# Kernel optimization log

Measured on AMD Instinct MI355X. Metric: run time of the kernel, lower is better.

Reference implementation:

```python
import jax, jax.numpy as jnp
import numpy as np

K = 5            # srn kernel size (kernels[0])
EPSILON = 1e-3   # epsilons -> SRN additive noise scale
BN_EPS = 1e-5
NUM_SLICES = 3
OUT_CH = 64
CLASSES = 5


def _unfold(x, k):
    # torch.nn.Unfold, padding=0: (B, C*k*k, L), channel-major then (kh, kw) row-major
    B, C, H, W = x.shape
    Ho, Wo = H - k + 1, W - k + 1
    cols = jnp.stack([x[:, :, i:i + Ho, j:j + Wo]
                      for i in range(k) for j in range(k)], axis=2)  # (B,C,k*k,Ho,Wo)
    return cols.reshape(B, C * k * k, Ho * Wo), Ho, Wo


def _bn(x, g, b):
    # BatchNorm2d in training mode: batch statistics, biased variance
    m = x.mean((0, 2, 3), keepdims=True)
    v = x.var((0, 2, 3), keepdims=True)
    return (x - m) * jax.lax.rsqrt(v + BN_EPS) * g[None, :, None, None] + b[None, :, None, None]


def _conv(x, w, b):
    y = jax.lax.conv_general_dilated(x, w, (1, 1), 'VALID',
                                     dimension_numbers=('NCHW', 'OIHW', 'NCHW'))
    return y + b[None, :, None, None]


def _avgpool(x, s):
    B, C, H, W = x.shape
    return x.reshape(B, C, H // s, s, W // s, s).mean((3, 5))


def _maxpool(x, s):
    B, C, H, W = x.shape
    return x.reshape(B, C, H // s, s, W // s, s).max((3, 5))


def _srn(x, srn_w):
    B = x.shape[0]
    y, Ho, Wo = _unfold(x, K)                               # (B, n, L)
    y = y + EPSILON * jax.random.normal(jax.random.key(42), y.shape, y.dtype)
    gg = jnp.std(y, axis=1, ddof=1, keepdims=True)          # torch.std is unbiased
    y = y / gg
    O, C, _, _, S = srn_w.shape
    n = C * K * K
    X = srn_w.reshape(O, n, S)
    X = jnp.concatenate([jnp.ones((O, n, 1), X.dtype), X], axis=2)   # (O, n, S+1)
    Xcov = jnp.einsum('onf,ong->ofg', X, X)                 # X^T X, (O, 4, 4)
    Xinv = jnp.linalg.inv(Xcov)
    M = jnp.einsum('ofg,ong->ofn', Xinv, X)
    Wc = jnp.einsum('ofn,bnl->bofl', M, y)
    pred = jnp.einsum('onf,bofl->bonl', X, Wc)              # fitted values (B,O,n,L)
    err = jnp.mean((y[:, None] - pred) ** 2, axis=2)        # (B,O,L)
    err = err.reshape(B, O, Ho, Wo)
    A = (jnp.exp(-err) - np.exp(-1.0)) / (1.0 - np.exp(-1.0))
    return A - 0.5


def setup_inputs() -> dict:
    key = jax.random.key(0)
    ks = jax.random.split(key, 12)
    x = jax.random.normal(ks[0], (4, 3, 64, 64), jnp.float32)
    # xavier-style init scaled up for numerical stability of the small-matrix inverse
    srn_w = 0.05 * jax.random.normal(ks[1], (OUT_CH, 3, K, K, NUM_SLICES), jnp.float32)
    conv2_w = 0.05 * jax.random.normal(ks[2], (128, 64, 3, 3), jnp.float32)
    conv2_b = 0.01 * jax.random.normal(ks[3], (128,), jnp.float32)
    conv3_w = 0.05 * jax.random.normal(ks[4], (128, 128, 3, 3), jnp.float32)
    conv3_b = 0.01 * jax.random.normal(ks[5], (128,), jnp.float32)
    conv4_w = 0.05 * jax.random.normal(ks[6], (128, 128, 3, 3), jnp.float32)
    conv4_b = 0.01 * jax.random.normal(ks[7], (128,), jnp.float32)
    bn1_g = jnp.ones((64,), jnp.float32); bn1_b = jnp.zeros((64,), jnp.float32)
    bn2_g = jnp.ones((128,), jnp.float32); bn2_b = jnp.zeros((128,), jnp.float32)
    bn3_g = jnp.ones((128,), jnp.float32); bn3_b = jnp.zeros((128,), jnp.float32)
    bn4_g = jnp.ones((128,), jnp.float32); bn4_b = jnp.zeros((128,), jnp.float32)
    fc2_w = 0.05 * jax.random.normal(ks[8], (CLASSES, 128, 1, 1), jnp.float32)
    fc2_b = 0.01 * jax.random.normal(ks[9], (CLASSES,), jnp.float32)
    return dict(x=x, srn_w=srn_w, conv2_w=conv2_w, conv2_b=conv2_b,
                conv3_w=conv3_w, conv3_b=conv3_b, conv4_w=conv4_w, conv4_b=conv4_b,
                bn1_g=bn1_g, bn1_b=bn1_b, bn2_g=bn2_g, bn2_b=bn2_b,
                bn3_g=bn3_g, bn3_b=bn3_b, bn4_g=bn4_g, bn4_b=bn4_b,
                fc2_w=fc2_w, fc2_b=fc2_b)


def reference(x, srn_w, conv2_w, conv2_b, conv3_w, conv3_b, conv4_w, conv4_b,
              bn1_g, bn1_b, bn2_g, bn2_b, bn3_g, bn3_b, bn4_g, bn4_b,
              fc2_w, fc2_b):
    h = _srn(x, srn_w)                                      # (B,64,60,60)
    h = _avgpool(h, 2)
    h = _bn(h, bn1_g, bn1_b)
    h = jax.nn.relu(_bn(_conv(h, conv2_w, conv2_b), bn2_g, bn2_b))
    h = _avgpool(h, 2)
    h = jax.nn.relu(_bn(_conv(h, conv3_w, conv3_b), bn3_g, bn3_b))
    h = _maxpool(h, 2)
    h = jax.nn.relu(_bn(_conv(h, conv4_w, conv4_b), bn4_g, bn4_b))
    h = _maxpool(h, 4)                                      # (B,128,1,1)
    flat = h.reshape(h.shape[0], -1)                        # (B,128)
    return flat @ fc2_w.reshape(CLASSES, -1).T + fc2_b      # 1x1 conv == matmul
```

## Files before the change

### kernel.cpp

```cpp
#include <hip/hip_runtime.h>
#include <math.h>

__device__ __align__(16) float g_G[64 * 16];
__device__ __align__(16) float g_Wp[64 * 240];
__device__ __align__(16) float g_w2p[9 * 2304 * 4];
__device__ __align__(16) float g_w3p[17 * 2304 * 4];
__device__ __align__(16) float g_w4p[8 * 4608 * 4];
__device__ float g_s1[64],  g_q1[64];
__device__ float g_s2[128], g_q2[128];
__device__ float g_s3[128], g_q3[128];
__device__ float g_s4[128], g_q4[128];
__device__ __align__(16) float g_h1[4 * 30 * 30 * 64];
__device__ __align__(16) float g_h2[4 * 14 * 14 * 4 * 128];
__device__ __align__(16) float g_h3[4 * 6 * 6 * 4 * 128];
__device__ __align__(16) float g_h4[4 * 16 * 128];

__global__ void k_prep(const float* __restrict__ srn_w, const float* __restrict__ w2,
                       const float* __restrict__ w3, const float* __restrict__ w4) {
    int t = threadIdx.x, bid = blockIdx.x;
    int gid = bid * 256 + t, gstride = 128 * 256;
    for (int i = gid; i < 14400; i += gstride) {
        int o = i / 225, j = i % 225, row = j / 15, col = j % 15;
        g_Wp[o * 240 + row * 16 + col] = srn_w[i];
    }
    for (int j = gid; j < 73728; j += gstride) {
        int c = j & 3, s4 = j >> 2;
        int sl = s4 % 36, tmp = s4 / 36, oc_l = tmp & 63, blk = tmp >> 6;
        int it = blk & 3, ocg = blk >> 2;
        int kw = sl % 3, icq = (sl / 3) & 3, kh = sl / 12;
        int ic = it * 16 + icq * 4 + c;
        g_w2p[j] = w2[((ocg * 64 + oc_l) * 64 + ic) * 9 + kh * 3 + kw];
    }
    for (int j = gid; j < 147456; j += gstride) {
        int c = j & 3, s4 = j >> 2;
        int sl = s4 % 36, tmp = s4 / 36, oc_l = tmp & 63, blk = tmp >> 6;
        int it = blk & 7, ocg = blk >> 3;
        int kw = sl % 3, icq = (sl / 3) & 3, kh = sl / 12;
        int ic = it * 16 + icq * 4 + c;
        g_w3p[j] = w3[((ocg * 64 + oc_l) * 128 + ic) * 9 + kh * 3 + kw];
    }
    for (int j = gid; j < 147456; j += gstride) {
        int c = j & 3, s4 = j >> 2;
        int sl = s4 % 72, tmp = s4 / 72, oc_l = tmp & 15, blkq = tmp >> 4;
        int icq = blkq & 3, ocg = blkq >> 2;
        int kw = sl % 3, icb = (sl / 3) & 7, kh = sl / 24;
        int ic = icq * 32 + icb * 4 + c;
        g_w4p[j] = w4[((ocg * 16 + oc_l) * 128 + ic) * 9 + kh * 3 + kw];
    }
    if (bid == 0) {
        if (t < 64) { g_s1[t] = 0.f; g_q1[t] = 0.f; }
        if (t < 128) {
            g_s2[t] = 0.f; g_q2[t] = 0.f;
            g_s3[t] = 0.f; g_q3[t] = 0.f;
            g_s4[t] = 0.f; g_q4[t] = 0.f;
        }
        if (t < 64) {
            int o = t;
            const float* w = srn_w + o * 225;
            float c01 = 0, c02 = 0, c03 = 0, c11 = 0, c12 = 0, c13 = 0,
                  c22 = 0, c23 = 0, c33 = 0;
            for (int n = 0; n < 75; n++) {
                float w1 = w[n * 3 + 0], w2v = w[n * 3 + 1], w3v = w[n * 3 + 2];
                c01 += w1; c02 += w2v; c03 += w3v;
                c11 += w1 * w1; c12 += w1 * w2v; c13 += w1 * w3v;
                c22 += w2v * w2v; c23 += w2v * w3v; c33 += w3v * w3v;
            }
            float A[4][8];
            A[0][0] = 75.f; A[0][1] = c01; A[0][2] = c02; A[0][3] = c03;
            A[1][0] = c01;  A[1][1] = c11; A[1][2] = c12; A[1][3] = c13;
            A[2][0] = c02;  A[2][1] = c12; A[2][2] = c22; A[2][3] = c23;
            A[3][0] = c03;  A[3][1] = c13; A[3][2] = c23; A[3][3] = c33;
            for (int i = 0; i < 4; i++)
                for (int j = 0; j < 4; j++) A[i][4 + j] = (i == j) ? 1.f : 0.f;
            for (int p = 0; p < 4; p++) {
                float ip = 1.f / A[p][p];
                for (int j = 0; j < 8; j++) A[p][j] *= ip;
                for (int i = 0; i < 4; i++) if (i != p) {
                    float f = A[i][p];
                    for (int j = 0; j < 8; j++) A[i][j] -= f * A[p][j];
                }
            }
            for (int i = 0; i < 4; i++)
                for (int j = 0; j < 4; j++) g_G[o * 16 + i * 4 + j] = A[i][4 + j];
        }
    }
}

__global__ __launch_bounds__(256) void k_srn(const float* __restrict__ x) {
    __shared__ __align__(16) float wlds[64 * 244];
    __shared__ __align__(16) float glds[64 * 20];
    __shared__ float xsm[648];
    __shared__ float part[2 * 15 * 66];
    __shared__ float redS[256], redQ[256];
    int blk = blockIdx.x;
    int b = blk / 60, rem = blk % 60, r = rem >> 1, ch = rem & 1;
    int t = threadIdx.x;

    float4 wreg[15];
#pragma unroll
    for (int k = 0; k < 15; k++) wreg[k] = ((const float4*)g_Wp)[k * 256 + t];
    float4 greg = ((const float4*)g_G)[t];
    float xr[3];
#pragma unroll
    for (int k = 0; k < 3; k++) {
        int i = t + k * 256;
        if (i < 648) {
            int c = i / 216, rm = i % 216, rr = rm / 36, col = rm % 36;
            int gc = ch * 30 + col; if (gc > 63) gc = 63;
            xr[k] = x[((b * 3 + c) * 64 + (2 * r + rr)) * 64 + gc];
        }
    }
#pragma unroll
    for (int k = 0; k < 15; k++) {
        int idx = k * 256 + t;
        *(float4*)&wlds[(idx / 60) * 244 + (idx % 60) * 4] = wreg[k];
    }
    *(float4*)&glds[(t >> 2) * 20 + (t & 3) * 4] = greg;
#pragma unroll
    for (int k = 0; k < 3; k++) { int i = t + k * 256; if (i < 648) xsm[i] = xr[k]; }
    __syncthreads();

    int w = t >> 6, o = t & 63;
    int rw = w & 1, cq = w >> 1, base = cq * 16;

    float z1[16], z2[16], z3[16], s[16], q[16];
#pragma unroll
    for (int i = 0; i < 16; i++) { z1[i] = 0; z2[i] = 0; z3[i] = 0; s[i] = 0; q[i] = 0; }

    for (int c = 0; c < 3; c++) {
#pragma unroll
        for (int kh = 0; kh < 5; kh++) {
            float xv[20];
#pragma unroll
            for (int k = 0; k < 20; k++) xv[k] = xsm[(c * 6 + rw + kh) * 36 + base + k];
            float wf[16];
            const float* wp = &wlds[o * 244 + (c * 5 + kh) * 16];
            *(float4*)&wf[0]  = *(const float4*)&wp[0];
            *(float4*)&wf[4]  = *(const float4*)&wp[4];
            *(float4*)&wf[8]  = *(const float4*)&wp[8];
            *(float4*)&wf[12] = *(const float4*)&wp[12];
#pragma unroll
            for (int kw = 0; kw < 5; kw++) {
                float w1 = wf[kw * 3], w2 = wf[kw * 3 + 1], w3 = wf[kw * 3 + 2];
#pragma unroll
                for (int i = 0; i < 16; i++) {
                    float v = xv[kw + i];
                    s[i] += v; q[i] += v * v;
                    z1[i] += w1 * v; z2[i] += w2 * v; z3[i] += w3 * v;
                }
            }
        }
    }

    float gm[16];
    {
        const float* gp = &glds[o * 20];
        *(float4*)&gm[0]  = *(const float4*)&gp[0];
        *(float4*)&gm[4]  = *(const float4*)&gp[4];
        *(float4*)&gm[8]  = *(const float4*)&gp[8];
        *(float4*)&gm[12] = *(const float4*)&gp[12];
    }
    const float C1 = 0.36787944117144233f;
    const float INV = 1.5819767068693265f;
#pragma unroll
    for (int pp = 0; pp < 8; pp++) {
        int pl = cq * 8 + pp;
        if (pl < 15) {
            float aa = 0.f;
#pragma unroll
            for (int e = 0; e < 2; e++) {
                int i = 2 * pp + e;
                float sum = s[i], sq = q[i];
                float gg2 = (sq - sum * sum * (1.f / 75.f)) * (1.f / 74.f);
                float zf[4] = { sum, z1[i], z2[i], z3[i] };
                float qf = 0.f;
#pragma unroll
                for (int f = 0; f < 4; f++) {
                    float acc = 0.f;
#pragma unroll
                    for (int h = 0; h < 4; h++) acc += gm[f * 4 + h] * zf[h];
                    qf += acc * zf[f];
                }
                float err = (sq - qf) / (75.f * gg2);
                aa += (expf(-err) - C1) * INV - 0.5f;
            }
            part[(rw * 15 + pl) * 66 + o] = 0.25f * aa;
        }
    }
    __syncthreads();

    int j = t >> 6;
    float ps = 0.f, pq = 0.f;
    for (int pl = j; pl < 15; pl += 4) {
        float v = part[pl * 66 + o] + part[(15 + pl) * 66 + o];
        g_h1[((b * 30 + r) * 30 + ch * 15 + pl) * 64 + o] = v;
        ps += v; pq += v * v;
    }
    redS[t] = ps; redQ[t] = pq;
    __syncthreads();
    if (t < 64) {
        atomicAdd(&g_s1[t], redS[t] + redS[64 + t] + redS[128 + t] + redS[192 + t]);
        atomicAdd(&g_q1[t], redQ[t] + redQ[64 + t] + redQ[128 + t] + redQ[192 + t]);
    }
}

__global__ __launch_bounds__(256) void k_conv2(const float* __restrict__ g1,
                                               const float* __restrict__ b1) {
    __shared__ __align__(16) float ws[64 * 148];
    __shared__ __align__(16) float xs[3 * 30 * 64];
    __shared__ float redS[256], redQ[256];
    int blk = blockIdx.x;
    int b = blk / 56, rem = blk % 56, oh = rem >> 1, ocg = rem & 1;
    int t = threadIdx.x;
    int oc_l = t & 63, qtr = t >> 6, owb = qtr * 7;

    {
        int icb = (t & 15) * 4;
        float4 S = *(const float4*)&g_s1[icb], Q = *(const float4*)&g_q1[icb];
        float4 G4 = *(const float4*)&g1[icb], B4 = *(const float4*)&b1[icb];
        float scv[4], shv[4];
        float mm[4] = { S.x, S.y, S.z, S.w }, qq[4] = { Q.x, Q.y, Q.z, Q.w };
        float gg[4] = { G4.x, G4.y, G4.z, G4.w }, bb[4] = { B4.x, B4.y, B4.z, B4.w };
#pragma unroll
        for (int c = 0; c < 4; c++) {
            float m = mm[c] * (1.f / 3600.f);
            float v = qq[c] * (1.f / 3600.f) - m * m;
            scv[c] = gg[c] * rsqrtf(v + 1e-5f);
            shv[c] = bb[c] - m * scv[c];
        }
        const float4* src4 = (const float4*)(g_h1 + (b * 900 + oh * 30) * 64);
        float4 xr[6];
#pragma unroll
        for (int k = 0; k < 6; k++) { int i4 = t + k * 256; if (i4 < 1440) xr[k] = src4[i4]; }
        const float4* wsrc0 = (const float4*)g_w2p;
        float4 wreg[9];
#pragma unroll
        for (int k = 0; k < 9; k++) wreg[k] = wsrc0[(ocg * 4) * 2304 + k * 256 + t];
#pragma unroll
        for (int k = 0; k < 6; k++) {
            int i4 = t + k * 256;
            if (i4 < 1440) {
                float4 v;
                v.x = xr[k].x * scv[0] + shv[0]; v.y = xr[k].y * scv[1] + shv[1];
                v.z = xr[k].z * scv[2] + shv[2]; v.w = xr[k].w * scv[3] + shv[3];
                *(float4*)&xs[i4 * 4] = v;
            }
        }
#pragma unroll
        for (int k = 0; k < 9; k++) {
            int idx = k * 256 + t;
            *(float4*)&ws[(idx / 36) * 148 + (idx % 36) * 4] = wreg[k];
        }
    }
    __syncthreads();

    float acc[7] = {0, 0, 0, 0, 0, 0, 0};
    const float4* wsrc = (const float4*)g_w2p + (ocg * 4) * 2304;
    for (int it = 0; it < 4; ++it) {
        float4 wreg[9];
        if (it < 3) {
#pragma unroll
            for (int k = 0; k < 9; k++) wreg[k] = wsrc[(it + 1) * 2304 + k * 256 + t];
        }
#pragma unroll 1
        for (int icq = 0; icq < 4; icq++) {
            int xoff = it * 16 + icq * 4;
#pragma unroll
            for (int kh = 0; kh < 3; kh++) {
                const float* wb = &ws[oc_l * 148 + (kh * 4 + icq) * 12];
                float4 w0 = *(const float4*)&wb[0];
                float4 w1 = *(const float4*)&wb[4];
                float4 w2v = *(const float4*)&wb[8];
                const float* xrow = &xs[(kh * 30 + owb) * 64 + xoff];
                float4 x0 = *(const float4*)&xrow[0];
                float4 x1 = *(const float4*)&xrow[64];
#pragma unroll
                for (int i = 0; i < 7; i++) {
                    float4 x2 = *(const float4*)&xrow[(i + 2) * 64];
                    acc[i] += w0.x * x0.x + w0.y * x0.y + w0.z * x0.z + w0.w * x0.w
                            + w1.x * x1.x + w1.y * x1.y + w1.z * x1.z + w1.w * x1.w
                            + w2v.x * x2.x + w2v.y * x2.y + w2v.z * x2.z + w2v.w * x2.w;
                    x0 = x1; x1 = x2;
                }
            }
        }
        if (it < 3) {
            __syncthreads();
#pragma unroll
            for (int k = 0; k < 9; k++) {
                int idx = k * 256 + t;
                *(float4*)&ws[(idx / 36) * 148 + (idx % 36) * 4] = wreg[k];
            }
            __syncthreads();
        }
    }
    int oc = ocg * 64 + oc_l;
    float ps = 0.f, pq = 0.f;
#pragma unroll
    for (int i = 0; i < 7; i++) {
        int ow = owb + i;
        g_h2[(((b * 14 + (oh >> 1)) * 14 + (ow >> 1)) * 4 + (oh & 1) * 2 + (ow & 1)) * 128 + oc] = acc[i];
        ps += acc[i]; pq += acc[i] * acc[i];
    }
    redS[t] = ps; redQ[t] = pq;
    __syncthreads();
    if (t < 64) {
        atomicAdd(&g_s2[ocg * 64 + t], redS[t] + redS[64 + t] + redS[128 + t] + redS[192 + t]);
        atomicAdd(&g_q2[ocg * 64 + t], redQ[t] + redQ[64 + t] + redQ[128 + t] + redQ[192 + t]);
    }
}

__global__ __launch_bounds__(256) void k_conv3(const float* __restrict__ g2,
                                               const float* __restrict__ b2) {
    __shared__ __align__(16) float ws[64 * 148];
    __shared__ __align__(16) float xs[3 * 14 * 128];
    __shared__ float redS[256], redQ[256];
    int blk = blockIdx.x;
    int b = blk / 24, rem = blk % 24, oh = rem >> 1, ocg = rem & 1;
    int t = threadIdx.x;
    int oc_l = t & 63, qtr = t >> 6, owb = qtr * 3;

    {
        int icb = (t & 31) * 4;
        float4 S = *(const float4*)&g_s2[icb], Q = *(const float4*)&g_q2[icb];
        float4 G4 = *(const float4*)&g2[icb], B4 = *(const float4*)&b2[icb];
        float scv[4], shv[4];
        float mm[4] = { S.x, S.y, S.z, S.w }, qq[4] = { Q.x, Q.y, Q.z, Q.w };
        float gg[4] = { G4.x, G4.y, G4.z, G4.w }, bb[4] = { B4.x, B4.y, B4.z, B4.w };
#pragma unroll
        for (int c = 0; c < 4; c++) {
            float m = mm[c] * (1.f / 3136.f);
            float v = qq[c] * (1.f / 3136.f) - m * m;
            scv[c] = gg[c] * rsqrtf(v + 1e-5f);
            shv[c] = bb[c] - m * scv[c];
        }
        const float4* wsrc0 = (const float4*)g_w3p;
        float4 wreg[9];
#pragma unroll
        for (int k = 0; k < 9; k++) wreg[k] = wsrc0[(ocg * 8) * 2304 + k * 256 + t];
        float4 va[6], vb[6], vc[6], vd[6];
#pragma unroll
        for (int k = 0; k < 6; k++) {
            int i4 = t + k * 256;
            if (i4 < 1344) {
                int px = (i4 >> 5) % 14, rr = i4 / 448;
                const float4* p0 = (const float4*)&g_h2[(((b * 14 + oh + rr) * 14 + px) * 4) * 128 + (i4 & 31) * 4];
                va[k] = p0[0]; vb[k] = p0[32]; vc[k] = p0[64]; vd[k] = p0[96];
            }
        }
#pragma unroll
        for (int k = 0; k < 9; k++) {
            int idx = k * 256 + t;
            *(float4*)&ws[(idx / 36) * 148 + (idx % 36) * 4] = wreg[k];
        }
#pragma unroll
        for (int k = 0; k < 6; k++) {
            int i4 = t + k * 256;
            if (i4 < 1344) {
                float4 o4;
                o4.x = 0.25f * (fmaxf(va[k].x * scv[0] + shv[0], 0.f) + fmaxf(vb[k].x * scv[0] + shv[0], 0.f)
                              + fmaxf(vc[k].x * scv[0] + shv[0], 0.f) + fmaxf(vd[k].x * scv[0] + shv[0], 0.f));
                o4.y = 0.25f * (fmaxf(va[k].y * scv[1] + shv[1], 0.f) + fmaxf(vb[k].y * scv[1] + shv[1], 0.f)
                              + fmaxf(vc[k].y * scv[1] + shv[1], 0.f) + fmaxf(vd[k].y * scv[1] + shv[1], 0.f));
                o4.z = 0.25f * (fmaxf(va[k].z * scv[2] + shv[2], 0.f) + fmaxf(vb[k].z * scv[2] + shv[2], 0.f)
                              + fmaxf(vc[k].z * scv[2] + shv[2], 0.f) + fmaxf(vd[k].z * scv[2] + shv[2], 0.f));
                o4.w = 0.25f * (fmaxf(va[k].w * scv[3] + shv[3], 0.f) + fmaxf(vb[k].w * scv[3] + shv[3], 0.f)
                              + fmaxf(vc[k].w * scv[3] + shv[3], 0.f) + fmaxf(vd[k].w * scv[3] + shv[3], 0.f));
                *(float4*)&xs[i4 * 4] = o4;
            }
        }
    }
    __syncthreads();

    float acc[3] = {0, 0, 0};
    const float4* wsrc = (const float4*)g_w3p + (ocg * 8) * 2304;
    for (int it = 0; it < 8; ++it) {
        float4 wreg[9];
        if (it < 7) {
#pragma unroll
            for (int k = 0; k < 9; k++) wreg[k] = wsrc[(it + 1) * 2304 + k * 256 + t];
        }
#pragma unroll 1
        for (int icq = 0; icq < 4; icq++) {
            int xoff = it * 16 + icq * 4;
#pragma unroll
            for (int kh = 0; kh < 3; kh++) {
                const float* wb = &ws[oc_l * 148 + (kh * 4 + icq) * 12];
                float4 w0 = *(const float4*)&wb[0];
                float4 w1 = *(const float4*)&wb[4];
                float4 w2v = *(const float4*)&wb[8];
                const float* xrow = &xs[(kh * 14 + owb) * 128 + xoff];
                float4 x0 = *(const float4*)&xrow[0];
                float4 x1 = *(const float4*)&xrow[128];
#pragma unroll
                for (int i = 0; i < 3; i++) {
                    float4 x2 = *(const float4*)&xrow[(i + 2) * 128];
                    acc[i] += w0.x * x0.x + w0.y * x0.y + w0.z * x0.z + w0.w * x0.w
                            + w1.x * x1.x + w1.y * x1.y + w1.z * x1.z + w1.w * x1.w
                            + w2v.x * x2.x + w2v.y * x2.y + w2v.z * x2.z + w2v.w * x2.w;
                    x0 = x1; x1 = x2;
                }
            }
        }
        if (it < 7) {
            __syncthreads();
#pragma unroll
            for (int k = 0; k < 9; k++) {
                int idx = k * 256 + t;
                *(float4*)&ws[(idx / 36) * 148 + (idx % 36) * 4] = wreg[k];
            }
            __syncthreads();
        }
    }
    int oc = ocg * 64 + oc_l;
    float ps = 0.f, pq = 0.f;
#pragma unroll
    for (int i = 0; i < 3; i++) {
        int ow = owb + i;
        g_h3[(((b * 6 + (oh >> 1)) * 6 + (ow >> 1)) * 4 + (oh & 1) * 2 + (ow & 1)) * 128 + oc] = acc[i];
        ps += acc[i]; pq += acc[i] * acc[i];
    }
    redS[t] = ps; redQ[t] = pq;
    __syncthreads();
    if (t < 64) {
        atomicAdd(&g_s3[ocg * 64 + t], redS[t] + redS[64 + t] + redS[128 + t] + redS[192 + t]);
        atomicAdd(&g_q3[ocg * 64 + t], redQ[t] + redQ[64 + t] + redQ[128 + t] + redQ[192 + t]);
    }
}

__global__ __launch_bounds__(256) void k_conv4(const float* __restrict__ g3,
                                               const float* __restrict__ b3) {
    __shared__ __align__(16) float ws[64 * 292];
    __shared__ __align__(16) float xs[3 * 6 * 128];
    __shared__ float red[256];
    int blk = blockIdx.x;
    int b = blk / 32, rem = blk % 32, oh = rem / 8, ocg = rem % 8;
    int t = threadIdx.x;
    int oc_l = t & 15, ow = (t >> 4) & 3, icq = t >> 6;

    {
        int icb = (t & 31) * 4;
        float4 S = *(const float4*)&g_s3[icb], Q = *(const float4*)&g_q3[icb];
        float4 G4 = *(const float4*)&g3[icb], B4 = *(const float4*)&b3[icb];
        float scv[4], shv[4];
        float mm[4] = { S.x, S.y, S.z, S.w }, qq[4] = { Q.x, Q.y, Q.z, Q.w };
        float gg[4] = { G4.x, G4.y, G4.z, G4.w }, bb[4] = { B4.x, B4.y, B4.z, B4.w };
#pragma unroll
        for (int c = 0; c < 4; c++) {
            float m = mm[c] * (1.f / 576.f);
            float v = qq[c] * (1.f / 576.f) - m * m;
            scv[c] = gg[c] * rsqrtf(v + 1e-5f);
            shv[c] = bb[c] - m * scv[c];
        }
        const float4* wsrc = (const float4*)g_w4p + ocg * 4608;
        float4 wreg[18];
#pragma unroll
        for (int k = 0; k < 18; k++) wreg[k] = wsrc[k * 256 + t];
        float4 va[3], vb[3], vc[3], vd[3];
#pragma unroll
        for (int k = 0; k < 3; k++) {
            int i4 = t + k * 256;
            if (i4 < 576) {
                int px = (i4 >> 5) % 6, rr = i4 / 192;
                const float4* p0 = (const float4*)&g_h3[(((b * 6 + oh + rr) * 6 + px) * 4) * 128 + (i4 & 31) * 4];
                va[k] = p0[0]; vb[k] = p0[32]; vc[k] = p0[64]; vd[k] = p0[96];
            }
        }
#pragma unroll
        for (int k = 0; k < 18; k++) {
            int idx = k * 256 + t;
            *(float4*)&ws[(idx / 72) * 292 + (idx % 72) * 4] = wreg[k];
        }
#pragma unroll
        for (int k = 0; k < 3; k++) {
            int i4 = t + k * 256;
            if (i4 < 576) {
                float4 o4;
                o4.x = fmaxf(fmaxf(fmaxf(va[k].x * scv[0] + shv[0], vb[k].x * scv[0] + shv[0]),
                                   fmaxf(vc[k].x * scv[0] + shv[0], vd[k].x * scv[0] + shv[0])), 0.f);
                o4.y = fmaxf(fmaxf(fmaxf(va[k].y * scv[1] + shv[1], vb[k].y * scv[1] + shv[1]),
                                   fmaxf(vc[k].y * scv[1] + shv[1], vd[k].y * scv[1] + shv[1])), 0.f);
                o4.z = fmaxf(fmaxf(fmaxf(va[k].z * scv[2] + shv[2], vb[k].z * scv[2] + shv[2]),
                                   fmaxf(vc[k].z * scv[2] + shv[2], vd[k].z * scv[2] + shv[2])), 0.f);
                o4.w = fmaxf(fmaxf(fmaxf(va[k].w * scv[3] + shv[3], vb[k].w * scv[3] + shv[3]),
                                   fmaxf(vc[k].w * scv[3] + shv[3], vd[k].w * scv[3] + shv[3])), 0.f);
                *(float4*)&xs[i4 * 4] = o4;
            }
        }
    }
    __syncthreads();

    float acc = 0.f;
    const float* wbase = &ws[(icq * 16 + oc_l) * 292];
#pragma unroll 1
    for (int icbq = 0; icbq < 8; icbq++) {
#pragma unroll
        for (int kh = 0; kh < 3; kh++) {
            const float* wb = &wbase[(kh * 8 + icbq) * 12];
            float4 w0 = *(const float4*)&wb[0];
            float4 w1 = *(const float4*)&wb[4];
            float4 w2v = *(const float4*)&wb[8];
            float4 x0 = *(const float4*)&xs[(kh * 6 + ow) * 128 + icq * 32 + icbq * 4];
            float4 x1 = *(const float4*)&xs[(kh * 6 + ow + 1) * 128 + icq * 32 + icbq * 4];
            float4 x2 = *(const float4*)&xs[(kh * 6 + ow + 2) * 128 + icq * 32 + icbq * 4];
            acc += w0.x * x0.x + w0.y * x0.y + w0.z * x0.z + w0.w * x0.w
                 + w1.x * x1.x + w1.y * x1.y + w1.z * x1.z + w1.w * x1.w
                 + w2v.x * x2.x + w2v.y * x2.y + w2v.z * x2.z + w2v.w * x2.w;
        }
    }
    red[t] = acc;
    __syncthreads();
    if (t < 64) {
        float v = red[t] + red[t + 64] + red[t + 128] + red[t + 192];
        int oc = ocg * 16 + (t & 15);
        g_h4[((b * 4 + oh) * 4 + (t >> 4)) * 128 + oc] = v;
        float ps = v + __shfl_xor(v, 16);  ps += __shfl_xor(ps, 32);
        float pv = v * v;
        float pq = pv + __shfl_xor(pv, 16); pq += __shfl_xor(pq, 32);
        if (t < 16) { atomicAdd(&g_s4[ocg * 16 + t], ps); atomicAdd(&g_q4[ocg * 16 + t], pq); }
    }
}

__global__ __launch_bounds__(256) void k_final(const float* __restrict__ g4,
                                               const float* __restrict__ b4,
                                               const float* __restrict__ fcw,
                                               const float* __restrict__ fcb,
                                               float* __restrict__ out) {
    __shared__ float sc[128], sh[128];
    __shared__ float pooled[4][128];
    int t = threadIdx.x;
    if (t < 128) {
        float m = g_s4[t] * (1.f / 64.f);
        float v = g_q4[t] * (1.f / 64.f) - m * m;
        float rs = rsqrtf(v + 1e-5f);
        sc[t] = g4[t] * rs; sh[t] = b4[t] - m * sc[t];
    }
    __syncthreads();
    for (int item = t; item < 512; item += 256) {
        int b = item >> 7, oc = item & 127;
        float s = sc[oc], h = sh[oc];
        float mx = 0.f;
#pragma unroll
        for (int k = 0; k < 16; k++) mx = fmaxf(mx, g_h4[(b * 16 + k) * 128 + oc] * s + h);
        pooled[b][oc] = mx;
    }
    __syncthreads();
    if (t < 20) {
        int b = t / 5, cls = t % 5;
        float acc = fcb[cls];
        const float* w = &fcw[cls * 128];
        for (int oc = 0; oc < 128; oc++) acc += pooled[b][oc] * w[oc];
        out[b * 5 + cls] = acc;
    }
}

extern "C" void kernel_launch(void* const* d_in, const int* in_sizes, int n_in,
                              void* d_out, int out_size, void* d_ws, size_t ws_size,
                              hipStream_t stream) {
    (void)in_sizes; (void)n_in; (void)out_size; (void)d_ws; (void)ws_size;
    const float* x     = (const float*)d_in[0];
    const float* srn_w = (const float*)d_in[1];
    const float* w2    = (const float*)d_in[2];
    const float* w3    = (const float*)d_in[4];
    const float* w4    = (const float*)d_in[6];
    const float* g1 = (const float*)d_in[8];  const float* b1 = (const float*)d_in[9];
    const float* g2 = (const float*)d_in[10]; const float* b2 = (const float*)d_in[11];
    const float* g3 = (const float*)d_in[12]; const float* b3 = (const float*)d_in[13];
    const float* g4 = (const float*)d_in[14]; const float* b4 = (const float*)d_in[15];
    const float* fcw = (const float*)d_in[16]; const float* fcb = (const float*)d_in[17];
    float* out = (float*)d_out;

    k_prep <<<dim3(128), dim3(256), 0, stream>>>(srn_w, w2, w3, w4);
    k_srn  <<<dim3(240), dim3(256), 0, stream>>>(x);
    k_conv2<<<dim3(224), dim3(256), 0, stream>>>(g1, b1);
    k_conv3<<<dim3(96),  dim3(256), 0, stream>>>(g2, b2);
    k_conv4<<<dim3(128), dim3(256), 0, stream>>>(g3, b3);
    k_final<<<dim3(1),   dim3(256), 0, stream>>>(g4, b4, fcw, fcb, out);
}
```

Measured before the change: 115.4 us.

## Fold weight-prep kernel into downstream stages and zero BN stats via memset

Removes the separate k_prep launch. Each weight repack now runs inside the kernel one stage earlier: w2 in k_srn, w3 in k_conv2, w4 in k_conv3. Every SRN block computes its own 4x4 Gram inverse from the weights it holds in LDS. The BN statistic accumulators move to the workspace and are cleared with hipMemsetAsync. This saves a launch and its serialization, but adds redundant per-block Gram work and extra global writes in kernels that were already busy. The memset is still a separate stream operation.

Result: faster. 111.2 us (-3.7%).

```diff
diff --git a/kernel.cpp b/kernel.cpp
--- a/kernel.cpp
+++ b/kernel.cpp
@@ -1,29 +1,26 @@
 #include <hip/hip_runtime.h>
 #include <math.h>
 
-__device__ __align__(16) float g_G[64 * 16];
-__device__ __align__(16) float g_Wp[64 * 240];
 __device__ __align__(16) float g_w2p[9 * 2304 * 4];
 __device__ __align__(16) float g_w3p[17 * 2304 * 4];
 __device__ __align__(16) float g_w4p[8 * 4608 * 4];
-__device__ float g_s1[64],  g_q1[64];
-__device__ float g_s2[128], g_q2[128];
-__device__ float g_s3[128], g_q3[128];
-__device__ float g_s4[128], g_q4[128];
 __device__ __align__(16) float g_h1[4 * 30 * 30 * 64];
 __device__ __align__(16) float g_h2[4 * 14 * 14 * 4 * 128];
 __device__ __align__(16) float g_h3[4 * 6 * 6 * 4 * 128];
 __device__ __align__(16) float g_h4[4 * 16 * 128];
 
-__global__ void k_prep(const float* __restrict__ srn_w, const float* __restrict__ w2,
-                       const float* __restrict__ w3, const float* __restrict__ w4) {
-    int t = threadIdx.x, bid = blockIdx.x;
-    int gid = bid * 256 + t, gstride = 128 * 256;
-    for (int i = gid; i < 14400; i += gstride) {
-        int o = i / 225, j = i % 225, row = j / 15, col = j % 15;
-        g_Wp[o * 240 + row * 16 + col] = srn_w[i];
-    }
-    for (int j = gid; j < 73728; j += gstride) {
+__global__ __launch_bounds__(256) void k_srn(const float* __restrict__ x,
+                                             const float* __restrict__ srn_w,
+                                             const float* __restrict__ w2,
+                                             float* __restrict__ stats) {
+    __shared__ __align__(16) float wlds[64 * 244];
+    __shared__ float xsm[648];
+    __shared__ float part[2 * 15 * 66];
+    __shared__ float redS[256], redQ[256];
+    int bid = blockIdx.x, t = threadIdx.x;
+    int b = bid / 60, rem = bid % 60, r = rem >> 1, ch = rem & 1;
+
+    for (int j = bid * 256 + t; j < 73728; j += 240 * 256) {
         int c = j & 3, s4 = j >> 2;
         int sl = s4 % 36, tmp = s4 / 36, oc_l = tmp & 63, blk = tmp >> 6;
         int it = blk & 3, ocg = blk >> 2;
@@ -31,75 +28,13 @@
         int ic = it * 16 + icq * 4 + c;
         g_w2p[j] = w2[((ocg * 64 + oc_l) * 64 + ic) * 9 + kh * 3 + kw];
     }
-    for (int j = gid; j < 147456; j += gstride) {
-        int c = j & 3, s4 = j >> 2;
-        int sl = s4 % 36, tmp = s4 / 36, oc_l = tmp & 63, blk = tmp >> 6;
-        int it = blk & 7, ocg = blk >> 3;
-        int kw = sl % 3, icq = (sl / 3) & 3, kh = sl / 12;
-        int ic = it * 16 + icq * 4 + c;
-        g_w3p[j] = w3[((ocg * 64 + oc_l) * 128 + ic) * 9 + kh * 3 + kw];
-    }
-    for (int j = gid; j < 147456; j += gstride) {
-        int c = j & 3, s4 = j >> 2;
-        int sl = s4 % 72, tmp = s4 / 72, oc_l = tmp & 15, blkq = tmp >> 4;
-        int icq = blkq & 3, ocg = blkq >> 2;
-        int kw = sl % 3, icb = (sl / 3) & 7, kh = sl / 24;
-        int ic = icq * 32 + icb * 4 + c;
-        g_w4p[j] = w4[((ocg * 16 + oc_l) * 128 + ic) * 9 + kh * 3 + kw];
-    }
-    if (bid == 0) {
-        if (t < 64) { g_s1[t] = 0.f; g_q1[t] = 0.f; }
-        if (t < 128) {
-            g_s2[t] = 0.f; g_q2[t] = 0.f;
-            g_s3[t] = 0.f; g_q3[t] = 0.f;
-            g_s4[t] = 0.f; g_q4[t] = 0.f;
-        }
-        if (t < 64) {
-            int o = t;
-            const float* w = srn_w + o * 225;
-            float c01 = 0, c02 = 0, c03 = 0, c11 = 0, c12 = 0, c13 = 0,
-                  c22 = 0, c23 = 0, c33 = 0;
-            for (int n = 0; n < 75; n++) {
-                float w1 = w[n * 3 + 0], w2v = w[n * 3 + 1], w3v = w[n * 3 + 2];
-                c01 += w1; c02 += w2v; c03 += w3v;
-                c11 += w1 * w1; c12 += w1 * w2v; c13 += w1 * w3v;
-                c22 += w2v * w2v; c23 += w2v * w3v; c33 += w3v * w3v;
-            }
-            float A[4][8];
-            A[0][0] = 75.f; A[0][1] = c01; A[0][2] = c02; A[0][3] = c03;
-            A[1][0] = c01;  A[1][1] = c11; A[1][2] = c12; A[1][3] = c13;
-            A[2][0] = c02;  A[2][1] = c12; A[2][2] = c22; A[2][3] = c23;
-            A[3][0] = c03;  A[3][1] = c13; A[3][2] = c23; A[3][3] = c33;
-            for (int i = 0; i < 4; i++)
-                for (int j = 0; j < 4; j++) A[i][4 + j] = (i == j) ? 1.f : 0.f;
-            for (int p = 0; p < 4; p++) {
-                float ip = 1.f / A[p][p];
-                for (int j = 0; j < 8; j++) A[p][j] *= ip;
-                for (int i = 0; i < 4; i++) if (i != p) {
-                    float f = A[i][p];
-                    for (int j = 0; j < 8; j++) A[i][j] -= f * A[p][j];
-                }
-            }
-            for (int i = 0; i < 4; i++)
-                for (int j = 0; j < 4; j++) g_G[o * 16 + i * 4 + j] = A[i][4 + j];
-        }
-    }
-}
-
-__global__ __launch_bounds__(256) void k_srn(const float* __restrict__ x) {
-    __shared__ __align__(16) float wlds[64 * 244];
-    __shared__ __align__(16) float glds[64 * 20];
-    __shared__ float xsm[648];
-    __shared__ float part[2 * 15 * 66];
-    __shared__ float redS[256], redQ[256];
-    int blk = blockIdx.x;
-    int b = blk / 60, rem = blk % 60, r = rem >> 1, ch = rem & 1;
-    int t = threadIdx.x;
-
-    float4 wreg[15];
-#pragma unroll
-    for (int k = 0; k < 15; k++) wreg[k] = ((const float4*)g_Wp)[k * 256 + t];
-    float4 greg = ((const float4*)g_G)[t];
+
+    float4 wr[15];
+#pragma unroll
+    for (int k = 0; k < 15; k++) {
+        int i4 = k * 256 + t;
+        if (i4 < 3600) wr[k] = ((const float4*)srn_w)[i4];
+    }
     float xr[3];
 #pragma unroll
     for (int k = 0; k < 3; k++) {
@@ -112,10 +47,16 @@
     }
 #pragma unroll
     for (int k = 0; k < 15; k++) {
-        int idx = k * 256 + t;
-        *(float4*)&wlds[(idx / 60) * 244 + (idx % 60) * 4] = wreg[k];
-    }
-    *(float4*)&glds[(t >> 2) * 20 + (t & 3) * 4] = greg;
+        int i4 = k * 256 + t;
+        if (i4 < 3600) {
+            float v[4] = { wr[k].x, wr[k].y, wr[k].z, wr[k].w };
+#pragma unroll
+            for (int e = 0; e < 4; e++) {
+                int i = i4 * 4 + e, o = i / 225, j = i % 225;
+                wlds[o * 244 + (j / 15) * 16 + (j % 15)] = v[e];
+            }
+        }
+    }
 #pragma unroll
     for (int k = 0; k < 3; k++) { int i = t + k * 256; if (i < 648) xsm[i] = xr[k]; }
     __syncthreads();
@@ -125,7 +66,7 @@
 
     float z1[16], z2[16], z3[16], s[16], q[16];
 #pragma unroll
-    for (int i = 0; i < 16; i++) { z1[i] = 0; z2[i] = 0; z3[i] = 0; s[i] = 0; q[i] = 0; }
+    for (int i = 0; i < 16; i++) { z1[i]=0; z2[i]=0; z3[i]=0; s[i]=0; q[i]=0; }
 
     for (int c = 0; c < 3; c++) {
 #pragma unroll
@@ -141,12 +82,12 @@
             *(float4*)&wf[12] = *(const float4*)&wp[12];
 #pragma unroll
             for (int kw = 0; kw < 5; kw++) {
-                float w1 = wf[kw * 3], w2 = wf[kw * 3 + 1], w3 = wf[kw * 3 + 2];
+                float w1 = wf[kw * 3], w2v = wf[kw * 3 + 1], w3v = wf[kw * 3 + 2];
 #pragma unroll
                 for (int i = 0; i < 16; i++) {
                     float v = xv[kw + i];
                     s[i] += v; q[i] += v * v;
-                    z1[i] += w1 * v; z2[i] += w2 * v; z3[i] += w3 * v;
+                    z1[i] += w1 * v; z2[i] += w2v * v; z3[i] += w3v * v;
                 }
             }
         }
@@ -154,12 +95,50 @@
 
     float gm[16];
     {
-        const float* gp = &glds[o * 20];
-        *(float4*)&gm[0]  = *(const float4*)&gp[0];
-        *(float4*)&gm[4]  = *(const float4*)&gp[4];
-        *(float4*)&gm[8]  = *(const float4*)&gp[8];
-        *(float4*)&gm[12] = *(const float4*)&gp[12];
-    }
+        float c01=0,c02=0,c03=0,c11=0,c12=0,c13=0,c22=0,c23=0,c33=0;
+#pragma unroll
+        for (int row = 0; row < 15; row++) {
+            float wf[16];
+            const float* wp = &wlds[o * 244 + row * 16];
+            *(float4*)&wf[0]  = *(const float4*)&wp[0];
+            *(float4*)&wf[4]  = *(const float4*)&wp[4];
+            *(float4*)&wf[8]  = *(const float4*)&wp[8];
+            *(float4*)&wf[12] = *(const float4*)&wp[12];
+#pragma unroll
+            for (int kw = 0; kw < 5; kw++) {
+                float w1 = wf[kw*3], w2v = wf[kw*3+1], w3v = wf[kw*3+2];
+                c01 += w1; c02 += w2v; c03 += w3v;
+                c11 += w1*w1; c12 += w1*w2v; c13 += w1*w3v;
+                c22 += w2v*w2v; c23 += w2v*w3v; c33 += w3v*w3v;
+            }
+        }
+        float A[4][8];
+        A[0][0]=75.f; A[0][1]=c01; A[0][2]=c02; A[0][3]=c03;
+        A[1][0]=c01;  A[1][1]=c11; A[1][2]=c12; A[1][3]=c13;
+        A[2][0]=c02;  A[2][1]=c12; A[2][2]=c22; A[2][3]=c23;
+        A[3][0]=c03;  A[3][1]=c13; A[3][2]=c23; A[3][3]=c33;
+#pragma unroll
+        for (int i = 0; i < 4; i++)
+#pragma unroll
+            for (int j = 0; j < 4; j++) A[i][4 + j] = (i == j) ? 1.f : 0.f;
+#pragma unroll
+        for (int p = 0; p < 4; p++) {
+            float ip = 1.f / A[p][p];
+#pragma unroll
+            for (int j = 0; j < 8; j++) A[p][j] *= ip;
+#pragma unroll
+            for (int i = 0; i < 4; i++) if (i != p) {
+                float f = A[i][p];
+#pragma unroll
+                for (int j = 0; j < 8; j++) A[i][j] -= f * A[p][j];
+            }
+        }
+#pragma unroll
+        for (int i = 0; i < 4; i++)
+#pragma unroll
+            for (int j = 0; j < 4; j++) gm[i * 4 + j] = A[i][4 + j];
+    }
+
     const float C1 = 0.36787944117144233f;
     const float INV = 1.5819767068693265f;
 #pragma unroll
@@ -199,13 +178,15 @@
     redS[t] = ps; redQ[t] = pq;
     __syncthreads();
     if (t < 64) {
-        atomicAdd(&g_s1[t], redS[t] + redS[64 + t] + redS[128 + t] + redS[192 + t]);
-        atomicAdd(&g_q1[t], redQ[t] + redQ[64 + t] + redQ[128 + t] + redQ[192 + t]);
+        atomicAdd(&stats[t],      redS[t] + redS[64 + t] + redS[128 + t] + redS[192 + t]);
+        atomicAdd(&stats[64 + t], redQ[t] + redQ[64 + t] + redQ[128 + t] + redQ[192 + t]);
     }
 }
 
-__global__ __launch_bounds__(256) void k_conv2(const float* __restrict__ g1,
-                                               const float* __restrict__ b1) {
+__global__ __launch_bounds__(256) void k_conv2(const float* __restrict__ w3,
+                                               const float* __restrict__ g1,
+                                               const float* __restrict__ b1,
+                                               float* __restrict__ stats) {
     __shared__ __align__(16) float ws[64 * 148];
     __shared__ __align__(16) float xs[3 * 30 * 64];
     __shared__ float redS[256], redQ[256];
@@ -214,9 +195,18 @@
     int t = threadIdx.x;
     int oc_l = t & 63, qtr = t >> 6, owb = qtr * 7;
 
+    for (int j = blk * 256 + t; j < 147456; j += 224 * 256) {
+        int c = j & 3, s4 = j >> 2;
+        int sl = s4 % 36, tmp = s4 / 36, oc2 = tmp & 63, bk = tmp >> 6;
+        int it = bk & 7, og = bk >> 3;
+        int kw = sl % 3, icq = (sl / 3) & 3, kh = sl / 12;
+        int ic = it * 16 + icq * 4 + c;
+        g_w3p[j] = w3[((og * 64 + oc2) * 128 + ic) * 9 + kh * 3 + kw];
+    }
+
     {
         int icb = (t & 15) * 4;
-        float4 S = *(const float4*)&g_s1[icb], Q = *(const float4*)&g_q1[icb];
+        float4 S = *(const float4*)&stats[icb], Q = *(const float4*)&stats[64 + icb];
         float4 G4 = *(const float4*)&g1[icb], B4 = *(const float4*)&b1[icb];
         float scv[4], shv[4];
         float mm[4] = { S.x, S.y, S.z, S.w }, qq[4] = { Q.x, Q.y, Q.z, Q.w };
@@ -305,13 +295,15 @@
     redS[t] = ps; redQ[t] = pq;
     __syncthreads();
     if (t < 64) {
-        atomicAdd(&g_s2[ocg * 64 + t], redS[t] + redS[64 + t] + redS[128 + t] + redS[192 + t]);
-        atomicAdd(&g_q2[ocg * 64 + t], redQ[t] + redQ[64 + t] + redQ[128 + t] + redQ[192 + t]);
+        atomicAdd(&stats[128 + ocg * 64 + t], redS[t] + redS[64 + t] + redS[128 + t] + redS[192 + t]);
+        atomicAdd(&stats[256 + ocg * 64 + t], redQ[t] + redQ[64 + t] + redQ[128 + t] + redQ[192 + t]);
     }
 }
 
-__global__ __launch_bounds__(256) void k_conv3(const float* __restrict__ g2,
-                                               const float* __restrict__ b2) {
+__global__ __launch_bounds__(256) void k_conv3(const float* __restrict__ w4,
+                                               const float* __restrict__ g2,
+                                               const float* __restrict__ b2,
+                                               float* __restrict__ stats) {
     __shared__ __align__(16) float ws[64 * 148];
     __shared__ __align__(16) float xs[3 * 14 * 128];
     __shared__ float redS[256], redQ[256];
@@ -320,9 +312,18 @@
     int t = threadIdx.x;
     int oc_l = t & 63, qtr = t >> 6, owb = qtr * 3;
 
+    for (int j = blk * 256 + t; j < 147456; j += 96 * 256) {
+        int c = j & 3, s4 = j >> 2;
+        int sl = s4 % 72, tmp = s4 / 72, oc2 = tmp & 15, blkq = tmp >> 4;
+        int icq = blkq & 3, og = blkq >> 2;
+        int kw = sl % 3, icb2 = (sl / 3) & 7, kh = sl / 24;
+        int ic = icq * 32 + icb2 * 4 + c;
+        g_w4p[j] = w4[((og * 16 + oc2) * 128 + ic) * 9 + kh * 3 + kw];
+    }
+
     {
         int icb = (t & 31) * 4;
-        float4 S = *(const float4*)&g_s2[icb], Q = *(const float4*)&g_q2[icb];
+        float4 S = *(const float4*)&stats[128 + icb], Q = *(const float4*)&stats[256 + icb];
         float4 G4 = *(const float4*)&g2[icb], B4 = *(const float4*)&b2[icb];
         float scv[4], shv[4];
         float mm[4] = { S.x, S.y, S.z, S.w }, qq[4] = { Q.x, Q.y, Q.z, Q.w };
@@ -338,14 +339,14 @@
         float4 wreg[9];
 #pragma unroll
         for (int k = 0; k < 9; k++) wreg[k] = wsrc0[(ocg * 8) * 2304 + k * 256 + t];
-        float4 va[6], vb[6], vc[6], vd[6];
+        float4 pa[6], pb[6], pc[6], pd[6];
 #pragma unroll
         for (int k = 0; k < 6; k++) {
             int i4 = t + k * 256;
             if (i4 < 1344) {
                 int px = (i4 >> 5) % 14, rr = i4 / 448;
                 const float4* p0 = (const float4*)&g_h2[(((b * 14 + oh + rr) * 14 + px) * 4) * 128 + (i4 & 31) * 4];
-                va[k] = p0[0]; vb[k] = p0[32]; vc[k] = p0[64]; vd[k] = p0[96];
+                pa[k] = p0[0]; pb[k] = p0[32]; pc[k] = p0[64]; pd[k] = p0[96];
             }
         }
 #pragma unroll
@@ -358,14 +359,14 @@
             int i4 = t + k * 256;
             if (i4 < 1344) {
                 float4 o4;
-                o4.x = 0.25f * (fmaxf(va[k].x * scv[0] + shv[0], 0.f) + fmaxf(vb[k].x * scv[0] + shv[0], 0.f)
-                              + fmaxf(vc[k].x * scv[0] + shv[0], 0.f) + fmaxf(vd[k].x * scv[0] + shv[0], 0.f));
-                o4.y = 0.25f * (fmaxf(va[k].y * scv[1] + shv[1], 0.f) + fmaxf(vb[k].y * scv[1] + shv[1], 0.f)
-                              + fmaxf(vc[k].y * scv[1] + shv[1], 0.f) + fmaxf(vd[k].y * scv[1] + shv[1], 0.f));
-                o4.z = 0.25f * (fmaxf(va[k].z * scv[2] + shv[2], 0.f) + fmaxf(vb[k].z * scv[2] + shv[2], 0.f)
-                              + fmaxf(vc[k].z * scv[2] + shv[2], 0.f) + fmaxf(vd[k].z * scv[2] + shv[2], 0.f));
-                o4.w = 0.25f * (fmaxf(va[k].w * scv[3] + shv[3], 0.f) + fmaxf(vb[k].w * scv[3] + shv[3], 0.f)
-                              + fmaxf(vc[k].w * scv[3] + shv[3], 0.f) + fmaxf(vd[k].w * scv[3] + shv[3], 0.f));
+                o4.x = 0.25f * (fmaxf(pa[k].x * scv[0] + shv[0], 0.f) + fmaxf(pb[k].x * scv[0] + shv[0], 0.f)
+                              + fmaxf(pc[k].x * scv[0] + shv[0], 0.f) + fmaxf(pd[k].x * scv[0] + shv[0], 0.f));
+                o4.y = 0.25f * (fmaxf(pa[k].y * scv[1] + shv[1], 0.f) + fmaxf(pb[k].y * scv[1] + shv[1], 0.f)
+                              + fmaxf(pc[k].y * scv[1] + shv[1], 0.f) + fmaxf(pd[k].y * scv[1] + shv[1], 0.f));
+                o4.z = 0.25f * (fmaxf(pa[k].z * scv[2] + shv[2], 0.f) + fmaxf(pb[k].z * scv[2] + shv[2], 0.f)
+                              + fmaxf(pc[k].z * scv[2] + shv[2], 0.f) + fmaxf(pd[k].z * scv[2] + shv[2], 0.f));
+                o4.w = 0.25f * (fmaxf(pa[k].w * scv[3] + shv[3], 0.f) + fmaxf(pb[k].w * scv[3] + shv[3], 0.f)
+                              + fmaxf(pc[k].w * scv[3] + shv[3], 0.f) + fmaxf(pd[k].w * scv[3] + shv[3], 0.f));
                 *(float4*)&xs[i4 * 4] = o4;
             }
         }
@@ -423,13 +424,14 @@
     redS[t] = ps; redQ[t] = pq;
     __syncthreads();
     if (t < 64) {
-        atomicAdd(&g_s3[ocg * 64 + t], redS[t] + redS[64 + t] + redS[128 + t] + redS[192 + t]);
-        atomicAdd(&g_q3[ocg * 64 + t], redQ[t] + redQ[64 + t] + redQ[128 + t] + redQ[192 + t]);
+        atomicAdd(&stats[384 + ocg * 64 + t], redS[t] + redS[64 + t] + redS[128 + t] + redS[192 + t]);
+        atomicAdd(&stats[512 + ocg * 64 + t], redQ[t] + redQ[64 + t] + redQ[128 + t] + redQ[192 + t]);
     }
 }
 
 __global__ __launch_bounds__(256) void k_conv4(const float* __restrict__ g3,
-                                               const float* __restrict__ b3) {
+                                               const float* __restrict__ b3,
+                                               float* __restrict__ stats) {
     __shared__ __align__(16) float ws[64 * 292];
     __shared__ __align__(16) float xs[3 * 6 * 128];
     __shared__ float red[256];
@@ -440,7 +442,7 @@
 
     {
         int icb = (t & 31) * 4;
-        float4 S = *(const float4*)&g_s3[icb], Q = *(const float4*)&g_q3[icb];
+        float4 S = *(const float4*)&stats[384 + icb], Q = *(const float4*)&stats[512 + icb];
         float4 G4 = *(const float4*)&g3[icb], B4 = *(const float4*)&b3[icb];
         float scv[4], shv[4];
         float mm[4] = { S.x, S.y, S.z, S.w }, qq[4] = { Q.x, Q.y, Q.z, Q.w };
@@ -456,14 +458,14 @@
         float4 wreg[18];
 #pragma unroll
         for (int k = 0; k < 18; k++) wreg[k] = wsrc[k * 256 + t];
-        float4 va[3], vb[3], vc[3], vd[3];
+        float4 pa[3], pb[3], pc[3], pd[3];
 #pragma unroll
         for (int k = 0; k < 3; k++) {
             int i4 = t + k * 256;
             if (i4 < 576) {
                 int px = (i4 >> 5) % 6, rr = i4 / 192;
                 const float4* p0 = (const float4*)&g_h3[(((b * 6 + oh + rr) * 6 + px) * 4) * 128 + (i4 & 31) * 4];
-                va[k] = p0[0]; vb[k] = p0[32]; vc[k] = p0[64]; vd[k] = p0[96];
+                pa[k] = p0[0]; pb[k] = p0[32]; pc[k] = p0[64]; pd[k] = p0[96];
             }
         }
 #pragma unroll
@@ -476,14 +478,14 @@
             int i4 = t + k * 256;
             if (i4 < 576) {
                 float4 o4;
-                o4.x = fmaxf(fmaxf(fmaxf(va[k].x * scv[0] + shv[0], vb[k].x * scv[0] + shv[0]),
-                                   fmaxf(vc[k].x * scv[0] + shv[0], vd[k].x * scv[0] + shv[0])), 0.f);
-                o4.y = fmaxf(fmaxf(fmaxf(va[k].y * scv[1] + shv[1], vb[k].y * scv[1] + shv[1]),
-                                   fmaxf(vc[k].y * scv[1] + shv[1], vd[k].y * scv[1] + shv[1])), 0.f);
-                o4.z = fmaxf(fmaxf(fmaxf(va[k].z * scv[2] + shv[2], vb[k].z * scv[2] + shv[2]),
-                                   fmaxf(vc[k].z * scv[2] + shv[2], vd[k].z * scv[2] + shv[2])), 0.f);
-                o4.w = fmaxf(fmaxf(fmaxf(va[k].w * scv[3] + shv[3], vb[k].w * scv[3] + shv[3]),
-                                   fmaxf(vc[k].w * scv[3] + shv[3], vd[k].w * scv[3] + shv[3])), 0.f);
+                o4.x = fmaxf(fmaxf(fmaxf(pa[k].x * scv[0] + shv[0], pb[k].x * scv[0] + shv[0]),
+                                   fmaxf(pc[k].x * scv[0] + shv[0], pd[k].x * scv[0] + shv[0])), 0.f);
+                o4.y = fmaxf(fmaxf(fmaxf(pa[k].y * scv[1] + shv[1], pb[k].y * scv[1] + shv[1]),
+                                   fmaxf(pc[k].y * scv[1] + shv[1], pd[k].y * scv[1] + shv[1])), 0.f);
+                o4.z = fmaxf(fmaxf(fmaxf(pa[k].z * scv[2] + shv[2], pb[k].z * scv[2] + shv[2]),
+                                   fmaxf(pc[k].z * scv[2] + shv[2], pd[k].z * scv[2] + shv[2])), 0.f);
+                o4.w = fmaxf(fmaxf(fmaxf(pa[k].w * scv[3] + shv[3], pb[k].w * scv[3] + shv[3]),
+                                   fmaxf(pc[k].w * scv[3] + shv[3], pd[k].w * scv[3] + shv[3])), 0.f);
                 *(float4*)&xs[i4 * 4] = o4;
             }
         }
@@ -517,7 +519,10 @@
         float ps = v + __shfl_xor(v, 16);  ps += __shfl_xor(ps, 32);
         float pv = v * v;
         float pq = pv + __shfl_xor(pv, 16); pq += __shfl_xor(pq, 32);
-        if (t < 16) { atomicAdd(&g_s4[ocg * 16 + t], ps); atomicAdd(&g_q4[ocg * 16 + t], pq); }
+        if (t < 16) {
+            atomicAdd(&stats[640 + ocg * 16 + t], ps);
+            atomicAdd(&stats[768 + ocg * 16 + t], pq);
+        }
     }
 }
 
@@ -525,13 +530,14 @@
                                                const float* __restrict__ b4,
                                                const float* __restrict__ fcw,
                                                const float* __restrict__ fcb,
+                                               const float* __restrict__ stats,
                                                float* __restrict__ out) {
     __shared__ float sc[128], sh[128];
     __shared__ float pooled[4][128];
     int t = threadIdx.x;
     if (t < 128) {
-        float m = g_s4[t] * (1.f / 64.f);
-        float v = g_q4[t] * (1.f / 64.f) - m * m;
+        float m = stats[640 + t] * (1.f / 64.f);
+        float v = stats[768 + t] * (1.f / 64.f) - m * m;
         float rs = rsqrtf(v + 1e-5f);
         sc[t] = g4[t] * rs; sh[t] = b4[t] - m * sc[t];
     }
@@ -557,7 +563,7 @@
 extern "C" void kernel_launch(void* const* d_in, const int* in_sizes, int n_in,
                               void* d_out, int out_size, void* d_ws, size_t ws_size,
                               hipStream_t stream) {
-    (void)in_sizes; (void)n_in; (void)out_size; (void)d_ws; (void)ws_size;
+    (void)in_sizes; (void)n_in; (void)out_size; (void)ws_size;
     const float* x     = (const float*)d_in[0];
     const float* srn_w = (const float*)d_in[1];
     const float* w2    = (const float*)d_in[2];
@@ -569,11 +575,12 @@
     const float* g4 = (const float*)d_in[14]; const float* b4 = (const float*)d_in[15];
     const float* fcw = (const float*)d_in[16]; const float* fcb = (const float*)d_in[17];
     float* out = (float*)d_out;
-
-    k_prep <<<dim3(128), dim3(256), 0, stream>>>(srn_w, w2, w3, w4);
-    k_srn  <<<dim3(240), dim3(256), 0, stream>>>(x);
-    k_conv2<<<dim3(224), dim3(256), 0, stream>>>(g1, b1);
-    k_conv3<<<dim3(96),  dim3(256), 0, stream>>>(g2, b2);
-    k_conv4<<<dim3(128), dim3(256), 0, stream>>>(g3, b3);
-    k_final<<<dim3(1),   dim3(256), 0, stream>>>(g4, b4, fcw, fcb, out);
+    float* stats = (float*)d_ws;
+
+    hipMemsetAsync(d_ws, 0, 4096, stream);
+    k_srn  <<<dim3(240), dim3(256), 0, stream>>>(x, srn_w, w2, stats);
+    k_conv2<<<dim3(224), dim3(256), 0, stream>>>(w3, g1, b1, stats);
+    k_conv3<<<dim3(96),  dim3(256), 0, stream>>>(w4, g2, b2, stats);
+    k_conv4<<<dim3(128), dim3(256), 0, stream>>>(g3, b3, stats);
+    k_final<<<dim3(1),   dim3(256), 0, stream>>>(g4, b4, fcw, fcb, stats, out);
 }
```
